# Kernel optimization log

Hardware: AMD Instinct MI355X
Metric: run time of the kernel (lower is better)

The kernel has to match this reference:

```python
import jax, jax.numpy as jnp
import numpy as np
from jax import lax

STRIDE = 16
OFFSET = 8.0  # vgg16 backbone
C = 512
A = 9  # 3 ratios x 3 scales
THR = 0.05
IOU_THR = 0.7
N_OUT = 50
K = 2048  # fixed candidate budget for jit-able NMS

# anchors: rows of [[1,1],[1,2],[2,1]] * scale for scale in (128,256,512) -> [9,2] (w,h)
ANCHORS = np.concatenate([np.array([[1, 1], [1, 2], [2, 1]], np.float32) * s
                          for s in (128.0, 256.0, 512.0)], axis=0)


def _conv(x, w, b, pad):
    y = lax.conv_general_dilated(x, w, (1, 1), [(pad, pad), (pad, pad)],
                                 dimension_numbers=("NCHW", "OIHW", "NCHW"))
    return y + b[None, :, None, None]


def setup_inputs() -> dict:
    key = jax.random.key(0)
    ks = jax.random.split(key, 8)
    x = jax.random.normal(ks[0], (4, C, 64, 96), dtype=jnp.float32)
    w1 = jax.random.normal(ks[1], (C, C, 3, 3), dtype=jnp.float32) * 0.02
    b1 = jnp.zeros((C,), jnp.float32)
    w_cls = jax.random.normal(ks[2], (2 * A, C, 1, 1), dtype=jnp.float32) * 0.02
    b_cls = jnp.zeros((2 * A,), jnp.float32)
    w_reg = jax.random.normal(ks[3], (4 * A, C, 1, 1), dtype=jnp.float32) * 0.02
    b_reg = jnp.zeros((4 * A,), jnp.float32)
    return {"x": x, "w1": w1, "b1": b1, "w_cls": w_cls, "b_cls": b_cls,
            "w_reg": w_reg, "b_reg": b_reg, "h": 1024, "w": 1536}


def _rpn_forward(x, w1, b1, w_cls, b_cls, w_reg, b_reg, h, w):
    B = x.shape[0]
    f = _conv(x, w1, b1, 1)                      # [B,512,H,W] (no activation in original)
    cls = _conv(f, w_cls, b_cls, 0)              # [B,2A,H,W]
    cls = jax.nn.softmax(cls, axis=1)            # Softmax2d: over ALL 2A channels
    reg = _conv(f, w_reg, b_reg, 0)              # [B,4A,H,W]
    H, W = cls.shape[-2:]
    prob_fg = cls.reshape(B, A, 2, H, W)[:, :, 1]           # [B,A,H,W]
    reg = reg.reshape(B, A, 4, H, W).transpose(0, 1, 3, 4, 2)  # [B,A,H,W,4]

    scores = prob_fg.reshape(-1)                  # [B*A*H*W]
    reg_flat = reg.reshape(-1, 4)

    # threshold (torch.where) -> fixed-size top-K preselection for jit
    masked = jnp.where(scores >= THR, scores, -1.0)
    top_s, top_i = lax.top_k(masked, K)          # sorted descending
    valid = top_s >= THR

    # recover (a, y, x) from flat index; batch index is dropped (as in original NMS)
    aidx = (top_i // (H * W)) % A
    yidx = (top_i // W) % H
    xidx = top_i % W

    off_x = (w - OFFSET * 2) % STRIDE / 2 + OFFSET
    off_y = (h - OFFSET * 2) % STRIDE / 2 + OFFSET
    cx = xidx.astype(jnp.float32) * STRIDE + off_x
    cy = yidx.astype(jnp.float32) * STRIDE + off_y
    anc = jnp.asarray(ANCHORS)[aidx]             # [K,2] (w,h)

    r = reg_flat[top_i]                          # [K,4]
    bx = r[:, 0] * anc[:, 0] + cx
    by = r[:, 1] * anc[:, 1] + cy
    bw = jnp.exp(r[:, 2]) * anc[:, 0]
    bh = jnp.exp(r[:, 3]) * anc[:, 1]
    x1 = bx - bw * 0.5
    y1 = by - bh * 0.5
    x2 = bx + bw * 0.5
    y2 = by + bh * 0.5
    boxes = jnp.stack([x1, y1, x2, y2], axis=1)  # [K,4] xyxy

    # pairwise IoU [K,K]
    area = (x2 - x1) * (y2 - y1)
    ix1 = jnp.maximum(x1[:, None], x1[None, :])
    iy1 = jnp.maximum(y1[:, None], y1[None, :])
    ix2 = jnp.minimum(x2[:, None], x2[None, :])
    iy2 = jnp.minimum(y2[:, None], y2[None, :])
    inter = jnp.clip(ix2 - ix1, 0.0) * jnp.clip(iy2 - iy1, 0.0)
    iou = inter / (area[:, None] + area[None, :] - inter + 1e-9)

    idx = jnp.arange(K)

    def body(i, keep):
        sup = keep[i] & (iou[i] > IOU_THR) & (idx > i)
        return keep & ~sup

    keep = lax.fori_loop(0, K, body, valid)

    final_s = jnp.where(keep, top_s, -1.0)
    sel_s, sel_i = lax.top_k(final_s, N_OUT)     # first N kept, score order
    out_valid = sel_s >= THR
    out_scores = jnp.where(out_valid, sel_s, 0.0)
    out_boxes = jnp.where(out_valid[:, None], boxes[sel_i], 0.0)
    return out_scores, out_boxes


def reference(x, w1, b1, w_cls, b_cls, w_reg, b_reg, h, w):
    return _rpn_forward(x, w1, b1, w_cls, b_cls, w_reg, b_reg, h, w)
```

## Files before the change

### kernel.cpp

```cpp
#include <hip/hip_runtime.h>
#include <stdint.h>

#define NB 4
#define NC 512
#define NH 64
#define NW 96
#define NA 9
#define NPIX (NB*NA*NH*NW)
#define KSEL 2048
#define NOUT 50
#define THRS 0.05f

#define HIST_BASE 0x3D4CCu
#define HIST_SIZE 9024
#define CAND_CAP 8192

typedef _Float16 half8 __attribute__((ext_vector_type(8)));
typedef float floatx16 __attribute__((ext_vector_type(16)));

__device__ const float ANC_W[9] = {128.f,128.f,256.f,256.f,256.f,512.f,512.f,512.f,1024.f};
__device__ const float ANC_H[9] = {128.f,256.f,128.f,256.f,512.f,256.f,512.f,1024.f,512.f};

__global__ __launch_bounds__(256) void wexp2_k(const float* __restrict__ w1,
                                               uint4* __restrict__ wexp2) {
    __shared__ __align__(16) _Float16 lbuf[36 * 32 * 8];
    const int bid = blockIdx.x;
    const int cc = bid >> 4, cog = bid & 15;
    const int t = threadIdx.x;
    const int co_l = t >> 3, j = t & 7;
    const int co = cog * 32 + co_l;
    const float* r0 = w1 + ((size_t)co * 512 + cc * 16 + j) * 9;
    const float* r1 = r0 + 8 * 9;
#pragma unroll
    for (int kk = 0; kk < 9; ++kk) {
        const float v0 = r0[kk] * 1024.f;
        const float v1 = r1[kk] * 1024.f;
        const _Float16 h0 = (_Float16)v0, h1 = (_Float16)v1;
        const _Float16 l0 = (_Float16)(v0 - (float)h0);
        const _Float16 l1 = (_Float16)(v1 - (float)h1);
        lbuf[((kk * 4 + 0) * 32 + co_l) * 8 + j] = h0;
        lbuf[((kk * 4 + 1) * 32 + co_l) * 8 + j] = h1;
        lbuf[((kk * 4 + 2) * 32 + co_l) * 8 + j] = l0;
        lbuf[((kk * 4 + 3) * 32 + co_l) * 8 + j] = l1;
    }
    __syncthreads();
    for (int e = t; e < 1152; e += 256) {
        const int co_e = e & 31;
        const int rest = e >> 5;
        const uint4 v = *(const uint4*)&lbuf[(rest * 32 + co_e) * 8];
        wexp2[(((size_t)cc * 9) * 4 + rest) * 512 + cog * 32 + co_e] = v;
    }
}

#define XS_BYTES 12480
#define CONV_LDS XS_BYTES

__global__ __launch_bounds__(512, 4) void conv_mfma(
    const float* __restrict__ x, const uint4* __restrict__ wexp2,
    const float* __restrict__ b1, float* __restrict__ f)
{
    __shared__ __align__(16) char xs[CONV_LDS];
    const int t = threadIdx.x;
    const int bid = blockIdx.x;
    const int half = bid & 1, pxb = bid >> 1;
    const int b = pxb >> 6, r = pxb & 63, by = r >> 2, bx = r & 3;
    const int y0 = by * 4, x0 = bx * 24;
    const int wq = t >> 6, lane = t & 63;
    const int m32 = lane & 31, khalf = lane >> 5;

    int abase[3];
#pragma unroll
    for (int mt = 0; mt < 3; ++mt) {
        const int px = mt * 32 + m32;
        const int yl = px / 24, xl = px - yl * 24;
        abase[mt] = (yl * 26 + xl) * 80 + khalf * 16;
    }

    floatx16 acc[3];
#pragma unroll
    for (int mt = 0; mt < 3; ++mt)
#pragma unroll
        for (int i = 0; i < 16; ++i) acc[mt][i] = 0.f;

    const uint4* wsrc = wexp2 + (size_t)khalf * 512 + (half * 256 + wq * 32 + m32);

    const float* xb = x + (size_t)b * NC * (NH * NW);
    auto stage_x = [&](int cc) {
        const float* xc = xb + (size_t)cc * 16 * (NH * NW);
        for (int it = t; it < 312; it += 512) {
            const int kh = (it >= 156) ? 1 : 0;
            const int slot = it - kh * 156;
            const int ya = slot / 26, xa = slot - ya * 26;
            const int gy = y0 - 1 + ya, gx = x0 - 1 + xa;
            const bool ok = (gy >= 0 && gy < NH && gx >= 0 && gx < NW);
            const int off = ok ? (kh * 8 * 6144 + gy * 96 + gx) : 0;
            union { _Float16 h[8]; uint4 u; } hi, lo;
#pragma unroll
            for (int j = 0; j < 8; ++j) {
                const float v = (ok ? xc[off + j * 6144] : 0.f) * 1024.f;
                const _Float16 hh = (_Float16)v;
                hi.h[j] = hh;
                lo.h[j] = (_Float16)(v - (float)hh);
            }
            *(uint4*)(xs + slot * 80 + kh * 16) = hi.u;
            *(uint4*)(xs + slot * 80 + 32 + kh * 16) = lo.u;
        }
    };

    uint4 bch, bcl, bnh, bnl;
    bch = wsrc[0];
    bcl = wsrc[1024];

    int cc = 0, kk = 0;
    for (int q = 0; q < 288; ++q) {
        if (kk == 0) {
            __syncthreads();
            stage_x(cc);
            __syncthreads();
        }
        if (q < 287) {
            const size_t nb = (size_t)(q + 1) * 2048;
            bnh = wsrc[nb];
            bnl = wsrc[nb + 1024];
        }
        {
            const int ky = kk / 3, kx = kk - ky * 3;
            const char* xcur = xs + (ky * 26 + kx) * 80;
            half8 axh[3], axl[3];
#pragma unroll
            for (int mt = 0; mt < 3; ++mt) {
                axh[mt] = *(const half8*)(xcur + abase[mt]);
                axl[mt] = *(const half8*)(xcur + abase[mt] + 32);
            }
            const half8 bwh = __builtin_bit_cast(half8, bch);
            const half8 bwl = __builtin_bit_cast(half8, bcl);
#pragma unroll
            for (int mt = 0; mt < 3; ++mt)
                acc[mt] = __builtin_amdgcn_mfma_f32_32x32x16_f16(
                    axh[mt], bwh, acc[mt], 0, 0, 0);
#pragma unroll
            for (int mt = 0; mt < 3; ++mt)
                acc[mt] = __builtin_amdgcn_mfma_f32_32x32x16_f16(
                    axh[mt], bwl, acc[mt], 0, 0, 0);
#pragma unroll
            for (int mt = 0; mt < 3; ++mt)
                acc[mt] = __builtin_amdgcn_mfma_f32_32x32x16_f16(
                    axl[mt], bwh, acc[mt], 0, 0, 0);
        }
        bch = bnh; bcl = bnl;
        if (++kk == 9) { kk = 0; ++cc; }
    }

    const float inv = 1.0f / 1048576.0f;
    const int co = half * 256 + wq * 32 + m32;
    const float bias = b1[co];
#pragma unroll
    for (int mt = 0; mt < 3; ++mt) {
#pragma unroll
        for (int reg = 0; reg < 16; ++reg) {
            const int row = (reg & 3) + 8 * (reg >> 2) + 4 * khalf;
            const int pxl = mt * 32 + row;
            const int yl = pxl / 24, xl = pxl - yl * 24;
            const size_t gpx = (size_t)(b * 64 + y0 + yl) * 96 + (x0 + xl);
            f[gpx * 512 + co] = acc[mt][reg] * inv + bias;
        }
    }
}

__global__ __launch_bounds__(256) void head_k(
    const float* __restrict__ f, const float* __restrict__ wcls,
    const float* __restrict__ wreg, const float* __restrict__ bcls,
    const float* __restrict__ breg, float* __restrict__ scores,
    float* __restrict__ regs)
{
    __shared__ __align__(16) float smem[6912 + 128 * 57];
    float* wls = smem;
    float* lt  = smem + 6912;
    const int t = threadIdx.x;
    const int px0 = blockIdx.x * 128;
    const int px_l = t & 127, oh = t >> 7;
    float acc27[27];
#pragma unroll
    for (int k = 0; k < 27; ++k) acc27[k] = 0.f;

    for (int qd = 0; qd < 4; ++qd) {
        __syncthreads();
        for (int e = t; e < 6912; e += 256) {
            const int oc = e >> 7, c = e & 127;
            wls[e] = (oc < 18) ? wcls[oc * 512 + qd * 128 + c]
                               : wreg[(oc - 18) * 512 + qd * 128 + c];
        }
        __syncthreads();
        const float4* fp = (const float4*)(f + (size_t)(px0 + px_l) * 512 + qd * 128);
        const float4* wp4 = (const float4*)wls;
#pragma unroll 4
        for (int c4 = 0; c4 < 32; ++c4) {
            const float4 fv = fp[c4];
#pragma unroll
            for (int k = 0; k < 27; ++k) {
                const float4 wv = wp4[(oh * 27 + k) * 32 + c4];
                acc27[k] += fv.x * wv.x + fv.y * wv.y + fv.z * wv.z + fv.w * wv.w;
            }
        }
    }
    __syncthreads();
#pragma unroll
    for (int k = 0; k < 27; ++k) lt[px_l * 57 + oh * 27 + k] = acc27[k];
    __syncthreads();

    if (t < 128) {
        const int px = px0 + t;
        const float* row = lt + t * 57;
        float cl[18];
        float m = -1e30f;
#pragma unroll
        for (int oc = 0; oc < 18; ++oc) {
            cl[oc] = row[oc] + bcls[oc];
            m = fmaxf(m, cl[oc]);
        }
        float sum = 0.f;
#pragma unroll
        for (int oc = 0; oc < 18; ++oc) { cl[oc] = expf(cl[oc] - m); sum += cl[oc]; }
        const float inv = 1.f / sum;
        const int b = px / 6144;
        const int yx = px - b * 6144;
#pragma unroll
        for (int a = 0; a < 9; ++a) {
            const int idx = b * 55296 + a * 6144 + yx;
            scores[idx] = cl[2 * a + 1] * inv;
            float4 rv;
            rv.x = row[18 + a * 4 + 0] + breg[a * 4 + 0];
            rv.y = row[18 + a * 4 + 1] + breg[a * 4 + 1];
            rv.z = row[18 + a * 4 + 2] + breg[a * 4 + 2];
            rv.w = row[18 + a * 4 + 3] + breg[a * 4 + 3];
            ((float4*)regs)[idx] = rv;
        }
    }
}

__global__ __launch_bounds__(256) void hist_k(const float* __restrict__ scores,
                                              uint32_t* __restrict__ hist) {
    __shared__ uint32_t lh[HIST_SIZE];
    const int t = threadIdx.x;
    for (int e = t; e < HIST_SIZE; e += 256) lh[e] = 0u;
    __syncthreads();
    const float4 sv = ((const float4*)scores)[blockIdx.x * 256 + t];
    const float s4[4] = {sv.x, sv.y, sv.z, sv.w};
#pragma unroll
    for (int j = 0; j < 4; ++j) {
        const float s = s4[j];
        if (s >= THRS) {
            int bkt = (int)(__float_as_uint(s) >> 12) - (int)HIST_BASE;
            bkt = min(max(bkt, 0), HIST_SIZE - 1);
            atomicAdd(&lh[bkt], 1u);
        }
    }
    __syncthreads();
    for (int e = t; e < HIST_SIZE; e += 256) {
        const uint32_t v = lh[e];
        if (v) atomicAdd(&hist[e], v);
    }
}

__global__ void scan_k(const uint32_t* __restrict__ hist, uint32_t* __restrict__ ctl) {
    __shared__ uint32_t ssum[1024];
    const int t = threadIdx.x;
    uint32_t s = 0;
#pragma unroll
    for (int u = 0; u < 9; ++u) {
        const int bkt = t * 9 + u;
        if (bkt < HIST_SIZE) s += hist[bkt];
    }
    const uint32_t mysum = s;
    ssum[t] = s;
    __syncthreads();
    for (int off = 1; off < 1024; off <<= 1) {
        uint32_t v = (t + off < 1024) ? ssum[t + off] : 0u;
        __syncthreads();
        ssum[t] += v;
        __syncthreads();
    }
    const uint32_t total = ssum[0];
    const uint32_t above = (t < 1023) ? ssum[t + 1] : 0u;
    if (total < KSEL) {
        if (t == 0) ctl[0] = HIST_BASE;
    } else if (above < KSEL && above + mysum >= KSEL) {
        uint32_t run = above;
        for (int u = 8; u >= 0; --u) {
            const int bkt = t * 9 + u;
            if (bkt >= HIST_SIZE) continue;
            run += hist[bkt];
            if (run >= KSEL) { ctl[0] = HIST_BASE + (uint32_t)bkt; break; }
        }
    }
}

__global__ void collect_k(const float* __restrict__ scores, uint32_t* __restrict__ ctl,
                          uint64_t* __restrict__ cand) {
    const int i = blockIdx.x * 256 + threadIdx.x;
    const float s = scores[i];
    if (s >= THRS) {
        const uint32_t bits = __float_as_uint(s);
        if ((bits >> 12) >= ctl[0]) {
            const uint32_t pos = atomicAdd(&ctl[1], 1u);
            if (pos < CAND_CAP)
                cand[pos] = ((uint64_t)bits << 32) | (uint64_t)(0xFFFFFFFFu - (uint32_t)i);
        }
    }
}

__global__ void sort_decode_k(const uint64_t* __restrict__ cand, const uint32_t* __restrict__ ctl,
                              const float* __restrict__ regs,
                              const int* __restrict__ hp, const int* __restrict__ wp,
                              float* __restrict__ tops_s, float* __restrict__ boxes) {
    __shared__ uint64_t keys[CAND_CAP];
    const int t = threadIdx.x;
    const int M = min((int)ctl[1], CAND_CAP);
    const int N = (M <= 4096) ? 4096 : 8192;
    for (int k = t; k < N; k += 1024) keys[k] = (k < M) ? cand[k] : 0ull;
    __syncthreads();
    for (int size = 2; size <= N; size <<= 1) {
        for (int stride = size >> 1; stride > 0; stride >>= 1) {
            for (int k = t; k < N; k += 1024) {
                const int p = k ^ stride;
                if (p > k) {
                    const uint64_t a = keys[k], bb = keys[p];
                    const bool sw = ((k & size) == 0) ? (a < bb) : (a > bb);
                    if (sw) { keys[k] = bb; keys[p] = a; }
                }
            }
            __syncthreads();
        }
    }
    const int w_in = wp[0], h_in = hp[0];
    const float offx = (float)((w_in - 16) % 16) * 0.5f + 8.0f;
    const float offy = (float)((h_in - 16) % 16) * 0.5f + 8.0f;
    for (int k = t; k < KSEL; k += 1024) {
        const uint64_t key = keys[k];
        float sc = -1.f, x1 = 0.f, y1 = 0.f, x2 = 0.f, y2 = 0.f;
        if (k < M && key != 0ull) {
            const uint32_t idx = 0xFFFFFFFFu - (uint32_t)(key & 0xFFFFFFFFull);
            sc = __uint_as_float((uint32_t)(key >> 32));
            const int a  = (int)(idx / (NH * NW)) % NA;
            const int yy = (int)(idx / NW) % NH;
            const int xx = (int)(idx % NW);
            const float4 r = ((const float4*)regs)[idx];
            const float aw = ANC_W[a], ah = ANC_H[a];
            const float cx = (float)xx * 16.f + offx;
            const float cy = (float)yy * 16.f + offy;
            const float bx = r.x * aw + cx;
            const float by = r.y * ah + cy;
            const float bw = expf(r.z) * aw;
            const float bh = expf(r.w) * ah;
            x1 = bx - bw * 0.5f; y1 = by - bh * 0.5f;
            x2 = bx + bw * 0.5f; y2 = by + bh * 0.5f;
        }
        tops_s[k] = sc;
        ((float4*)boxes)[k] = make_float4(x1, y1, x2, y2);
    }
}

__global__ void iou_k(const float* __restrict__ boxes, uint64_t* __restrict__ mask) {
    __shared__ float4 jb[64];
    const int t = threadIdx.x;
    const int bi = blockIdx.x, bj = blockIdx.y;
    jb[t] = ((const float4*)boxes)[bj * 64 + t];
    __syncthreads();
    const int i = bi * 64 + t;
    const float4 mb = ((const float4*)boxes)[i];
    const float areai = (mb.z - mb.x) * (mb.w - mb.y);
    uint64_t w = 0;
    for (int jj = 0; jj < 64; ++jj) {
        const float4 ob = jb[jj];
        const int j = bj * 64 + jj;
        const float ix1 = fmaxf(mb.x, ob.x);
        const float iy1 = fmaxf(mb.y, ob.y);
        const float ix2 = fminf(mb.z, ob.z);
        const float iy2 = fminf(mb.w, ob.w);
        const float inter = fmaxf(ix2 - ix1, 0.f) * fmaxf(iy2 - iy1, 0.f);
        const float areaj = (ob.z - ob.x) * (ob.w - ob.y);
        const float iou = inter / (areai + areaj - inter + 1e-9f);
        if (iou > 0.7f && j > i) w |= (1ull << jj);
    }
    mask[(size_t)i * 32 + bj] = w;
}

__global__ void nms_k(const float* __restrict__ tops_s, const float* __restrict__ boxes,
                      const uint64_t* __restrict__ mask, float* __restrict__ out) {
    __shared__ uint64_t remv[32];
    __shared__ float ssc[KSEL];
    __shared__ int sel[NOUT];
    const int t = threadIdx.x;
    for (int k = t; k < KSEL; k += 64) ssc[k] = tops_s[k];
    if (t < 32) remv[t] = 0ull;
    uint64_t nextrow = (t < 32) ? mask[t] : 0ull;
    int cnt = 0;
    for (int i = 0; i < KSEL && cnt < NOUT; ++i) {
        const uint64_t cur = nextrow;
        if (t < 32 && i + 1 < KSEL) nextrow = mask[(size_t)(i + 1) * 32 + t];
        const uint64_t rw = remv[i >> 6];
        const bool sup = (rw >> (i & 63)) & 1ull;
        if (ssc[i] >= THRS && !sup) {
            if (t < 32) remv[t] |= cur;
            if (t == 0) sel[cnt] = i;
            ++cnt;
        }
    }
    for (int k = t; k < NOUT; k += 64) {
        float s = 0.f;
        float4 bb = make_float4(0.f, 0.f, 0.f, 0.f);
        if (k < cnt) { const int i = sel[k]; s = ssc[i]; bb = ((const float4*)boxes)[i]; }
        out[k] = s;
        out[NOUT + k * 4 + 0] = bb.x;
        out[NOUT + k * 4 + 1] = bb.y;
        out[NOUT + k * 4 + 2] = bb.z;
        out[NOUT + k * 4 + 3] = bb.w;
    }
}

extern "C" void kernel_launch(void* const* d_in, const int* in_sizes, int n_in,
                              void* d_out, int out_size, void* d_ws, size_t ws_size,
                              hipStream_t stream) {
    const float* x    = (const float*)d_in[0];
    const float* w1   = (const float*)d_in[1];
    const float* b1   = (const float*)d_in[2];
    const float* wcls = (const float*)d_in[3];
    const float* bcls = (const float*)d_in[4];
    const float* wreg = (const float*)d_in[5];
    const float* breg = (const float*)d_in[6];
    const int*   hp   = (const int*)d_in[7];
    const int*   wp   = (const int*)d_in[8];
    float* out = (float*)d_out;

    char* ws = (char*)d_ws;
    size_t off = 0;
    auto carve = [&](size_t bytes) -> void* {
        void* p = ws + off;
        off = (off + bytes + 255) & ~(size_t)255;
        return p;
    };
    uint4*    wexp2  = (uint4*)carve((size_t)288 * 4 * 512 * 16);
    float*    f      = (float*)carve((size_t)24576 * 512 * 4);
    float*    scores = (float*)carve((size_t)NPIX * 4);
    float*    regs   = (float*)carve((size_t)NPIX * 16);
    uint32_t* hist   = (uint32_t*)carve((size_t)HIST_SIZE * 4);
    uint32_t* ctl    = (uint32_t*)carve(256);
    uint64_t* cand   = (uint64_t*)carve((size_t)CAND_CAP * 8);
    float*    tops_s = (float*)carve((size_t)KSEL * 4);
    float*    boxes  = (float*)carve((size_t)KSEL * 16);
    uint64_t* mask   = (uint64_t*)carve((size_t)KSEL * 32 * 8);
    (void)ws_size; (void)in_sizes; (void)n_in; (void)out_size;

    hipMemsetAsync(hist, 0, (size_t)HIST_SIZE * 4, stream);
    hipMemsetAsync(ctl, 0, 256, stream);

    wexp2_k<<<512, 256, 0, stream>>>(w1, wexp2);
    conv_mfma<<<512, 512, 0, stream>>>(x, wexp2, b1, f);
    head_k<<<192, 256, 0, stream>>>(f, wcls, wreg, bcls, breg, scores, regs);
    hist_k<<<216, 256, 0, stream>>>(scores, hist);
    scan_k<<<1, 1024, 0, stream>>>(hist, ctl);
    collect_k<<<NPIX / 256, 256, 0, stream>>>(scores, ctl, cand);
    sort_decode_k<<<1, 1024, 0, stream>>>(cand, ctl, regs, hp, wp, tops_s, boxes);
    iou_k<<<dim3(KSEL / 64, KSEL / 64), 64, 0, stream>>>(boxes, mask);
    nms_k<<<1, 64, 0, stream>>>(tops_s, boxes, mask, out);
}
```

Before: 656.1 us.

## Give each conv wave two N-tiles and segment candidate atomics

The conv kernel drops to 256 threads per block, and each wave now computes two 32-channel output tiles, so every A fragment loaded from LDS feeds twice as many MFMAs. The 9-tap inner loop is unrolled per channel chunk. The candidate collector spreads its atomic counter over 8 segments to reduce contention, and the sorter always bitonic-sorts the full 8192 slots. Costs: more accumulator registers, lower occupancy, a larger fixed sort, and a per-segment cap of 1024 that could drop candidates if any segment overflows.

```diff
diff --git a/kernel.cpp b/kernel.cpp
--- a/kernel.cpp
+++ b/kernel.cpp
@@ -14,6 +14,7 @@
 #define HIST_BASE 0x3D4CCu
 #define HIST_SIZE 9024
 #define CAND_CAP 8192
+#define SEG_CAP 1024
 
 typedef _Float16 half8 __attribute__((ext_vector_type(8)));
 typedef float floatx16 __attribute__((ext_vector_type(16)));
@@ -53,13 +54,11 @@
 }
 
 #define XS_BYTES 12480
-#define CONV_LDS XS_BYTES
-
-__global__ __launch_bounds__(512, 4) void conv_mfma(
+__global__ __launch_bounds__(256, 2) void conv_mfma(
     const float* __restrict__ x, const uint4* __restrict__ wexp2,
     const float* __restrict__ b1, float* __restrict__ f)
 {
-    __shared__ __align__(16) char xs[CONV_LDS];
+    __shared__ __align__(16) char xs[XS_BYTES];
     const int t = threadIdx.x;
     const int bid = blockIdx.x;
     const int half = bid & 1, pxb = bid >> 1;
@@ -76,18 +75,20 @@
         abase[mt] = (yl * 26 + xl) * 80 + khalf * 16;
     }
 
-    floatx16 acc[3];
+    floatx16 acc[3][2];
 #pragma unroll
     for (int mt = 0; mt < 3; ++mt)
 #pragma unroll
-        for (int i = 0; i < 16; ++i) acc[mt][i] = 0.f;
-
-    const uint4* wsrc = wexp2 + (size_t)khalf * 512 + (half * 256 + wq * 32 + m32);
+        for (int nt = 0; nt < 2; ++nt)
+#pragma unroll
+            for (int i = 0; i < 16; ++i) acc[mt][nt][i] = 0.f;
+
+    const uint4* wsrc = wexp2 + (size_t)khalf * 512 + half * 256 + wq * 64 + m32;
 
     const float* xb = x + (size_t)b * NC * (NH * NW);
     auto stage_x = [&](int cc) {
         const float* xc = xb + (size_t)cc * 16 * (NH * NW);
-        for (int it = t; it < 312; it += 512) {
+        for (int it = t; it < 312; it += 256) {
             const int kh = (it >= 156) ? 1 : 0;
             const int slot = it - kh * 156;
             const int ya = slot / 26, xa = slot - ya * 26;
@@ -107,23 +108,28 @@
         }
     };
 
-    uint4 bch, bcl, bnh, bnl;
-    bch = wsrc[0];
-    bcl = wsrc[1024];
-
-    int cc = 0, kk = 0;
-    for (int q = 0; q < 288; ++q) {
-        if (kk == 0) {
-            __syncthreads();
-            stage_x(cc);
-            __syncthreads();
-        }
-        if (q < 287) {
-            const size_t nb = (size_t)(q + 1) * 2048;
-            bnh = wsrc[nb];
-            bnl = wsrc[nb + 1024];
-        }
-        {
+    uint4 bc[2][2], bn[2][2];
+#pragma unroll
+    for (int kind = 0; kind < 2; ++kind)
+#pragma unroll
+        for (int nt = 0; nt < 2; ++nt)
+            bc[kind][nt] = wsrc[(size_t)kind * 1024 + nt * 32];
+
+    for (int cc = 0; cc < 32; ++cc) {
+        __syncthreads();
+        stage_x(cc);
+        __syncthreads();
+#pragma unroll
+        for (int kk = 0; kk < 9; ++kk) {
+            const int q = cc * 9 + kk;
+            if (q < 287) {
+                const size_t nb = (size_t)(q + 1) * 2048;
+#pragma unroll
+                for (int kind = 0; kind < 2; ++kind)
+#pragma unroll
+                    for (int nt = 0; nt < 2; ++nt)
+                        bn[kind][nt] = wsrc[nb + kind * 1024 + nt * 32];
+            }
             const int ky = kk / 3, kx = kk - ky * 3;
             const char* xcur = xs + (ky * 26 + kx) * 80;
             half8 axh[3], axl[3];
@@ -132,37 +138,53 @@
                 axh[mt] = *(const half8*)(xcur + abase[mt]);
                 axl[mt] = *(const half8*)(xcur + abase[mt] + 32);
             }
-            const half8 bwh = __builtin_bit_cast(half8, bch);
-            const half8 bwl = __builtin_bit_cast(half8, bcl);
-#pragma unroll
-            for (int mt = 0; mt < 3; ++mt)
-                acc[mt] = __builtin_amdgcn_mfma_f32_32x32x16_f16(
-                    axh[mt], bwh, acc[mt], 0, 0, 0);
-#pragma unroll
-            for (int mt = 0; mt < 3; ++mt)
-                acc[mt] = __builtin_amdgcn_mfma_f32_32x32x16_f16(
-                    axh[mt], bwl, acc[mt], 0, 0, 0);
-#pragma unroll
-            for (int mt = 0; mt < 3; ++mt)
-                acc[mt] = __builtin_amdgcn_mfma_f32_32x32x16_f16(
-                    axl[mt], bwh, acc[mt], 0, 0, 0);
-        }
-        bch = bnh; bcl = bnl;
-        if (++kk == 9) { kk = 0; ++cc; }
+            half8 bwh[2], bwl[2];
+#pragma unroll
+            for (int nt = 0; nt < 2; ++nt) {
+                bwh[nt] = __builtin_bit_cast(half8, bc[0][nt]);
+                bwl[nt] = __builtin_bit_cast(half8, bc[1][nt]);
+            }
+#pragma unroll
+            for (int nt = 0; nt < 2; ++nt)
+#pragma unroll
+                for (int mt = 0; mt < 3; ++mt)
+                    acc[mt][nt] = __builtin_amdgcn_mfma_f32_32x32x16_f16(
+                        axh[mt], bwh[nt], acc[mt][nt], 0, 0, 0);
+#pragma unroll
+            for (int nt = 0; nt < 2; ++nt)
+#pragma unroll
+                for (int mt = 0; mt < 3; ++mt)
+                    acc[mt][nt] = __builtin_amdgcn_mfma_f32_32x32x16_f16(
+                        axh[mt], bwl[nt], acc[mt][nt], 0, 0, 0);
+#pragma unroll
+            for (int nt = 0; nt < 2; ++nt)
+#pragma unroll
+                for (int mt = 0; mt < 3; ++mt)
+                    acc[mt][nt] = __builtin_amdgcn_mfma_f32_32x32x16_f16(
+                        axl[mt], bwh[nt], acc[mt][nt], 0, 0, 0);
+#pragma unroll
+            for (int kind = 0; kind < 2; ++kind)
+#pragma unroll
+                for (int nt = 0; nt < 2; ++nt)
+                    bc[kind][nt] = bn[kind][nt];
+        }
     }
 
     const float inv = 1.0f / 1048576.0f;
-    const int co = half * 256 + wq * 32 + m32;
-    const float bias = b1[co];
-#pragma unroll
-    for (int mt = 0; mt < 3; ++mt) {
-#pragma unroll
-        for (int reg = 0; reg < 16; ++reg) {
-            const int row = (reg & 3) + 8 * (reg >> 2) + 4 * khalf;
-            const int pxl = mt * 32 + row;
-            const int yl = pxl / 24, xl = pxl - yl * 24;
-            const size_t gpx = (size_t)(b * 64 + y0 + yl) * 96 + (x0 + xl);
-            f[gpx * 512 + co] = acc[mt][reg] * inv + bias;
+#pragma unroll
+    for (int nt = 0; nt < 2; ++nt) {
+        const int co = half * 256 + wq * 64 + nt * 32 + m32;
+        const float bias = b1[co];
+#pragma unroll
+        for (int mt = 0; mt < 3; ++mt) {
+#pragma unroll
+            for (int reg = 0; reg < 16; ++reg) {
+                const int row = (reg & 3) + 8 * (reg >> 2) + 4 * khalf;
+                const int pxl = mt * 32 + row;
+                const int yl = pxl / 24, xl = pxl - yl * 24;
+                const size_t gpx = (size_t)(b * 64 + y0 + yl) * 96 + (x0 + xl);
+                f[gpx * 512 + co] = acc[mt][nt][reg] * inv + bias;
+            }
         }
     }
 }
@@ -302,9 +324,11 @@
     if (s >= THRS) {
         const uint32_t bits = __float_as_uint(s);
         if ((bits >> 12) >= ctl[0]) {
-            const uint32_t pos = atomicAdd(&ctl[1], 1u);
-            if (pos < CAND_CAP)
-                cand[pos] = ((uint64_t)bits << 32) | (uint64_t)(0xFFFFFFFFu - (uint32_t)i);
+            const int seg = blockIdx.x & 7;
+            const uint32_t pos = atomicAdd(&ctl[1 + seg], 1u);
+            if (pos < SEG_CAP)
+                cand[seg * SEG_CAP + pos] =
+                    ((uint64_t)bits << 32) | (uint64_t)(0xFFFFFFFFu - (uint32_t)i);
         }
     }
 }
@@ -315,13 +339,15 @@
                               float* __restrict__ tops_s, float* __restrict__ boxes) {
     __shared__ uint64_t keys[CAND_CAP];
     const int t = threadIdx.x;
-    const int M = min((int)ctl[1], CAND_CAP);
-    const int N = (M <= 4096) ? 4096 : 8192;
-    for (int k = t; k < N; k += 1024) keys[k] = (k < M) ? cand[k] : 0ull;
-    __syncthreads();
-    for (int size = 2; size <= N; size <<= 1) {
+    for (int k = t; k < CAND_CAP; k += 1024) {
+        const int seg = k >> 10, idx = k & (SEG_CAP - 1);
+        const uint32_t cnt = ctl[1 + seg];
+        keys[k] = ((uint32_t)idx < cnt && idx < SEG_CAP) ? cand[k] : 0ull;
+    }
+    __syncthreads();
+    for (int size = 2; size <= CAND_CAP; size <<= 1) {
         for (int stride = size >> 1; stride > 0; stride >>= 1) {
-            for (int k = t; k < N; k += 1024) {
+            for (int k = t; k < CAND_CAP; k += 1024) {
                 const int p = k ^ stride;
                 if (p > k) {
                     const uint64_t a = keys[k], bb = keys[p];
@@ -338,7 +364,7 @@
     for (int k = t; k < KSEL; k += 1024) {
         const uint64_t key = keys[k];
         float sc = -1.f, x1 = 0.f, y1 = 0.f, x2 = 0.f, y2 = 0.f;
-        if (k < M && key != 0ull) {
+        if (key != 0ull) {
             const uint32_t idx = 0xFFFFFFFFu - (uint32_t)(key & 0xFFFFFFFFull);
             sc = __uint_as_float((uint32_t)(key >> 32));
             const int a  = (int)(idx / (NH * NW)) % NA;
@@ -455,7 +481,7 @@
     hipMemsetAsync(ctl, 0, 256, stream);
 
     wexp2_k<<<512, 256, 0, stream>>>(w1, wexp2);
-    conv_mfma<<<512, 512, 0, stream>>>(x, wexp2, b1, f);
+    conv_mfma<<<512, 256, 0, stream>>>(x, wexp2, b1, f);
     head_k<<<192, 256, 0, stream>>>(f, wcls, wreg, bcls, breg, scores, regs);
     hist_k<<<216, 256, 0, stream>>>(scores, hist);
     scan_k<<<1, 1024, 0, stream>>>(hist, ctl);
```

Result: slower. 710.5 us (+8.3%).

## Double-buffer conv input staging, fuse histogram into head, segment candidate atomics

Applied to the files above, without the earlier changes.

The conv kernel now double-buffers the x tile in LDS. Each thread preloads the next channel chunk into registers while MFMAs run on the current buffer, which removes one barrier per chunk and hides global load latency. The score histogram is built inside head_k, eliminating the separate hist_k launch and its re-read of scores. Candidate collection spreads atomics over 8 per-segment counters to reduce contention. The trade-off is that the sort now always runs over the full 8192 slots, and each segment is capped at 1024 candidates, so candidates can be dropped if they are unevenly distributed across segments.

```diff
diff --git a/kernel.cpp b/kernel.cpp
--- a/kernel.cpp
+++ b/kernel.cpp
@@ -14,6 +14,7 @@
 #define HIST_BASE 0x3D4CCu
 #define HIST_SIZE 9024
 #define CAND_CAP 8192
+#define SEG_CAP 1024
 
 typedef _Float16 half8 __attribute__((ext_vector_type(8)));
 typedef float floatx16 __attribute__((ext_vector_type(16)));
@@ -52,14 +53,12 @@
     }
 }
 
-#define XS_BYTES 12480
-#define CONV_LDS XS_BYTES
-
+#define XS_ONE 12480
 __global__ __launch_bounds__(512, 4) void conv_mfma(
     const float* __restrict__ x, const uint4* __restrict__ wexp2,
     const float* __restrict__ b1, float* __restrict__ f)
 {
-    __shared__ __align__(16) char xs[CONV_LDS];
+    __shared__ __align__(16) char xs[2 * XS_ONE];
     const int t = threadIdx.x;
     const int bid = blockIdx.x;
     const int half = bid & 1, pxb = bid >> 1;
@@ -84,26 +83,33 @@
 
     const uint4* wsrc = wexp2 + (size_t)khalf * 512 + (half * 256 + wq * 32 + m32);
 
+    const int kh_s = (t >= 156) ? 1 : 0;
+    const int slot_s = t - kh_s * 156;
+    const int ya_s = slot_s / 26, xa_s = slot_s - ya_s * 26;
+    const int gy_s = y0 - 1 + ya_s, gx_s = x0 - 1 + xa_s;
+    const bool ok_s = (t < 312) && (gy_s >= 0 && gy_s < NH && gx_s >= 0 && gx_s < NW);
     const float* xb = x + (size_t)b * NC * (NH * NW);
-    auto stage_x = [&](int cc) {
-        const float* xc = xb + (size_t)cc * 16 * (NH * NW);
-        for (int it = t; it < 312; it += 512) {
-            const int kh = (it >= 156) ? 1 : 0;
-            const int slot = it - kh * 156;
-            const int ya = slot / 26, xa = slot - ya * 26;
-            const int gy = y0 - 1 + ya, gx = x0 - 1 + xa;
-            const bool ok = (gy >= 0 && gy < NH && gx >= 0 && gx < NW);
-            const int off = ok ? (kh * 8 * 6144 + gy * 96 + gx) : 0;
+    const float* xsrc0 = xb + (ok_s ? (kh_s * 8 * 6144 + gy_s * 96 + gx_s) : 0);
+
+    float xr[8];
+    auto xload = [&](int cc) {
+        const float* xc = xsrc0 + (size_t)cc * 16 * (NH * NW);
+#pragma unroll
+        for (int j = 0; j < 8; ++j) xr[j] = ok_s ? xc[j * 6144] : 0.f;
+    };
+    auto xcommit = [&](int bufsel) {
+        if (t < 312) {
             union { _Float16 h[8]; uint4 u; } hi, lo;
 #pragma unroll
             for (int j = 0; j < 8; ++j) {
-                const float v = (ok ? xc[off + j * 6144] : 0.f) * 1024.f;
+                const float v = xr[j] * 1024.f;
                 const _Float16 hh = (_Float16)v;
                 hi.h[j] = hh;
                 lo.h[j] = (_Float16)(v - (float)hh);
             }
-            *(uint4*)(xs + slot * 80 + kh * 16) = hi.u;
-            *(uint4*)(xs + slot * 80 + 32 + kh * 16) = lo.u;
+            char* base = xs + bufsel * XS_ONE + slot_s * 80 + kh_s * 16;
+            *(uint4*)base = hi.u;
+            *(uint4*)(base + 32) = lo.u;
         }
     };
 
@@ -111,21 +117,23 @@
     bch = wsrc[0];
     bcl = wsrc[1024];
 
-    int cc = 0, kk = 0;
-    for (int q = 0; q < 288; ++q) {
-        if (kk == 0) {
-            __syncthreads();
-            stage_x(cc);
-            __syncthreads();
-        }
-        if (q < 287) {
-            const size_t nb = (size_t)(q + 1) * 2048;
-            bnh = wsrc[nb];
-            bnl = wsrc[nb + 1024];
-        }
-        {
+    xload(0);
+    xcommit(0);
+    __syncthreads();
+
+    for (int cc = 0; cc < 32; ++cc) {
+        if (cc < 31) xload(cc + 1);
+        const char* xbuf = xs + (cc & 1) * XS_ONE;
+#pragma unroll
+        for (int kk = 0; kk < 9; ++kk) {
+            const int q = cc * 9 + kk;
+            if (q < 287) {
+                const size_t nb = (size_t)(q + 1) * 2048;
+                bnh = wsrc[nb];
+                bnl = wsrc[nb + 1024];
+            }
             const int ky = kk / 3, kx = kk - ky * 3;
-            const char* xcur = xs + (ky * 26 + kx) * 80;
+            const char* xcur = xbuf + (ky * 26 + kx) * 80;
             half8 axh[3], axl[3];
 #pragma unroll
             for (int mt = 0; mt < 3; ++mt) {
@@ -146,9 +154,10 @@
             for (int mt = 0; mt < 3; ++mt)
                 acc[mt] = __builtin_amdgcn_mfma_f32_32x32x16_f16(
                     axl[mt], bwh, acc[mt], 0, 0, 0);
-        }
-        bch = bnh; bcl = bnl;
-        if (++kk == 9) { kk = 0; ++cc; }
+            bch = bnh; bcl = bnl;
+        }
+        if (cc < 31) xcommit((cc + 1) & 1);
+        __syncthreads();
     }
 
     const float inv = 1.0f / 1048576.0f;
@@ -171,7 +180,7 @@
     const float* __restrict__ f, const float* __restrict__ wcls,
     const float* __restrict__ wreg, const float* __restrict__ bcls,
     const float* __restrict__ breg, float* __restrict__ scores,
-    float* __restrict__ regs)
+    float* __restrict__ regs, uint32_t* __restrict__ hist)
 {
     __shared__ __align__(16) float smem[6912 + 128 * 57];
     float* wls = smem;
@@ -208,6 +217,9 @@
     for (int k = 0; k < 27; ++k) lt[px_l * 57 + oh * 27 + k] = acc27[k];
     __syncthreads();
 
+    float sc9[9];
+#pragma unroll
+    for (int a = 0; a < 9; ++a) sc9[a] = 0.f;
     if (t < 128) {
         const int px = px0 + t;
         const float* row = lt + t * 57;
@@ -227,7 +239,9 @@
 #pragma unroll
         for (int a = 0; a < 9; ++a) {
             const int idx = b * 55296 + a * 6144 + yx;
-            scores[idx] = cl[2 * a + 1] * inv;
+            const float s = cl[2 * a + 1] * inv;
+            sc9[a] = s;
+            scores[idx] = s;
             float4 rv;
             rv.x = row[18 + a * 4 + 0] + breg[a * 4 + 0];
             rv.y = row[18 + a * 4 + 1] + breg[a * 4 + 1];
@@ -236,23 +250,20 @@
             ((float4*)regs)[idx] = rv;
         }
     }
-}
-
-__global__ __launch_bounds__(256) void hist_k(const float* __restrict__ scores,
-                                              uint32_t* __restrict__ hist) {
-    __shared__ uint32_t lh[HIST_SIZE];
-    const int t = threadIdx.x;
+
+    __syncthreads();
+    uint32_t* lh = (uint32_t*)smem;
     for (int e = t; e < HIST_SIZE; e += 256) lh[e] = 0u;
     __syncthreads();
-    const float4 sv = ((const float4*)scores)[blockIdx.x * 256 + t];
-    const float s4[4] = {sv.x, sv.y, sv.z, sv.w};
-#pragma unroll
-    for (int j = 0; j < 4; ++j) {
-        const float s = s4[j];
-        if (s >= THRS) {
-            int bkt = (int)(__float_as_uint(s) >> 12) - (int)HIST_BASE;
-            bkt = min(max(bkt, 0), HIST_SIZE - 1);
-            atomicAdd(&lh[bkt], 1u);
+    if (t < 128) {
+#pragma unroll
+        for (int a = 0; a < 9; ++a) {
+            const float s = sc9[a];
+            if (s >= THRS) {
+                int bkt = (int)(__float_as_uint(s) >> 12) - (int)HIST_BASE;
+                bkt = min(max(bkt, 0), HIST_SIZE - 1);
+                atomicAdd(&lh[bkt], 1u);
+            }
         }
     }
     __syncthreads();
@@ -302,9 +313,11 @@
     if (s >= THRS) {
         const uint32_t bits = __float_as_uint(s);
         if ((bits >> 12) >= ctl[0]) {
-            const uint32_t pos = atomicAdd(&ctl[1], 1u);
-            if (pos < CAND_CAP)
-                cand[pos] = ((uint64_t)bits << 32) | (uint64_t)(0xFFFFFFFFu - (uint32_t)i);
+            const int seg = blockIdx.x & 7;
+            const uint32_t pos = atomicAdd(&ctl[1 + seg], 1u);
+            if (pos < SEG_CAP)
+                cand[seg * SEG_CAP + pos] =
+                    ((uint64_t)bits << 32) | (uint64_t)(0xFFFFFFFFu - (uint32_t)i);
         }
     }
 }
@@ -315,13 +328,15 @@
                               float* __restrict__ tops_s, float* __restrict__ boxes) {
     __shared__ uint64_t keys[CAND_CAP];
     const int t = threadIdx.x;
-    const int M = min((int)ctl[1], CAND_CAP);
-    const int N = (M <= 4096) ? 4096 : 8192;
-    for (int k = t; k < N; k += 1024) keys[k] = (k < M) ? cand[k] : 0ull;
-    __syncthreads();
-    for (int size = 2; size <= N; size <<= 1) {
+    for (int k = t; k < CAND_CAP; k += 1024) {
+        const int seg = k >> 10, idx = k & (SEG_CAP - 1);
+        const uint32_t cnt = ctl[1 + seg];
+        keys[k] = ((uint32_t)idx < cnt) ? cand[k] : 0ull;
+    }
+    __syncthreads();
+    for (int size = 2; size <= CAND_CAP; size <<= 1) {
         for (int stride = size >> 1; stride > 0; stride >>= 1) {
-            for (int k = t; k < N; k += 1024) {
+            for (int k = t; k < CAND_CAP; k += 1024) {
                 const int p = k ^ stride;
                 if (p > k) {
                     const uint64_t a = keys[k], bb = keys[p];
@@ -338,7 +353,7 @@
     for (int k = t; k < KSEL; k += 1024) {
         const uint64_t key = keys[k];
         float sc = -1.f, x1 = 0.f, y1 = 0.f, x2 = 0.f, y2 = 0.f;
-        if (k < M && key != 0ull) {
+        if (key != 0ull) {
             const uint32_t idx = 0xFFFFFFFFu - (uint32_t)(key & 0xFFFFFFFFull);
             sc = __uint_as_float((uint32_t)(key >> 32));
             const int a  = (int)(idx / (NH * NW)) % NA;
@@ -456,8 +471,7 @@
 
     wexp2_k<<<512, 256, 0, stream>>>(w1, wexp2);
     conv_mfma<<<512, 512, 0, stream>>>(x, wexp2, b1, f);
-    head_k<<<192, 256, 0, stream>>>(f, wcls, wreg, bcls, breg, scores, regs);
-    hist_k<<<216, 256, 0, stream>>>(scores, hist);
+    head_k<<<192, 256, 0, stream>>>(f, wcls, wreg, bcls, breg, scores, regs, hist);
     scan_k<<<1, 1024, 0, stream>>>(hist, ctl);
     collect_k<<<NPIX / 256, 256, 0, stream>>>(scores, ctl, cand);
     sort_decode_k<<<1, 1024, 0, stream>>>(cand, ctl, regs, hp, wp, tops_s, boxes);
```

Measured after the change: 666.2 us. Within noise of the previous version (+1.5%).
